# Performance work log

Hardware: AMD Instinct MI355X
Metric: run time of the kernel (lower is better)

Reference implementation:

```python
import jax, jax.numpy as jnp
import numpy as np

WS = 8          # window size
DIM = 512       # channels
NH = 16         # heads
HD = DIM // NH  # head dim = 32
N = WS * WS     # tokens per window = 64
NW = 64         # windows per image
B = 16          # images
BW = B * NW     # total windows = 1024
SCALE = HD ** -0.5


def _relative_position_index():
    # Swin relative position index, shape (N, N), values in [0, (2*WS-1)^2)
    coords = np.stack(np.meshgrid(np.arange(WS), np.arange(WS), indexing='ij'))  # (2, WS, WS)
    coords_flat = coords.reshape(2, -1)                                           # (2, N)
    rel = coords_flat[:, :, None] - coords_flat[:, None, :]                       # (2, N, N)
    rel = rel.transpose(1, 2, 0).astype(np.int32)                                 # (N, N, 2)
    rel[:, :, 0] += WS - 1
    rel[:, :, 1] += WS - 1
    rel[:, :, 0] *= 2 * WS - 1
    return jnp.asarray(rel.sum(-1))                                               # (N, N)


def setup_inputs() -> dict:
    key = jax.random.key(0)
    ks = jax.random.split(key, 7)
    x = jax.random.normal(ks[0], (BW, N, DIM), dtype=jnp.float32)
    mask = jax.random.normal(ks[1], (NW, N, N), dtype=jnp.float32)  # shift mask (additive)
    qkv_w = jax.random.normal(ks[2], (3 * DIM, DIM), dtype=jnp.float32) * 0.02
    qkv_b = jax.random.normal(ks[3], (3 * DIM,), dtype=jnp.float32) * 0.02
    rel_bias_table = jax.random.normal(ks[4], ((2 * WS - 1) ** 2, NH), dtype=jnp.float32) * 0.02
    proj_w = jax.random.normal(ks[5], (DIM, DIM), dtype=jnp.float32) * 0.02
    proj_b = jax.random.normal(ks[6], (DIM,), dtype=jnp.float32) * 0.02
    rel_index = _relative_position_index()
    return {"x": x, "mask": mask, "qkv_w": qkv_w, "qkv_b": qkv_b,
            "rel_bias_table": rel_bias_table, "proj_w": proj_w, "proj_b": proj_b,
            "rel_index": rel_index}


def reference(x, mask, qkv_w, qkv_b, rel_bias_table, proj_w, proj_b, rel_index):
    # qkv projection: (BW, N, 3*DIM) -> (3, BW, NH, N, HD)
    qkv = (x @ qkv_w.T + qkv_b).reshape(BW, N, 3, NH, HD).transpose(2, 0, 3, 1, 4)
    q, k, v = qkv[0], qkv[1], qkv[2]
    # scaled dot-product scores: (BW, NH, N, N)
    attn = jnp.einsum('bhnd,bhmd->bhnm', q * SCALE, k)
    # relative position bias: gather (N*N,) -> (N, N, NH) -> (NH, N, N)
    bias = rel_bias_table[rel_index.reshape(-1)].reshape(N, N, NH).transpose(2, 0, 1)
    attn = attn + bias[None]
    # shift mask: broadcast over images and heads
    attn = attn.reshape(B, NW, NH, N, N) + mask[None, :, None]
    attn = jax.nn.softmax(attn.reshape(BW, NH, N, N), axis=-1)
    # weighted values: (BW, NH, N, HD) -> (BW, N, DIM)
    out = jnp.einsum('bhnm,bhmd->bhnd', attn, v).transpose(0, 2, 1, 3).reshape(BW, N, DIM)
    return out @ proj_w.T + proj_b
```

## Files before the change

kernel.cpp:

```cpp
#include <hip/hip_runtime.h>
#include <hip/hip_bf16.h>

typedef __bf16 bf16;
typedef __bf16 bf16x4 __attribute__((ext_vector_type(4)));
typedef __bf16 bf16x8 __attribute__((ext_vector_type(8)));
typedef float  f32x4  __attribute__((ext_vector_type(4)));

#define AS1 __attribute__((address_space(1)))
#define AS3 __attribute__((address_space(3)))

__device__ __forceinline__ void gld_lds16(const void* g, void* l) {
    __builtin_amdgcn_global_load_lds((AS1 void*)g, (AS3 void*)l, 16, 0, 0);
}

__global__ void cvt_kernel(const float* __restrict__ in, bf16* __restrict__ out,
                           int n4) {
    for (long i = (long)blockIdx.x * blockDim.x + threadIdx.x; i < n4;
         i += (long)gridDim.x * blockDim.x) {
        f32x4 v = ((const f32x4*)in)[i];
        bf16x4 h;
#pragma unroll
        for (int e = 0; e < 4; ++e) h[e] = (bf16)v[e];
        ((bf16x4*)out)[i] = h;
    }
}

__global__ void bias_kernel(const int* __restrict__ rel_index,
                            const float* __restrict__ table,
                            float* __restrict__ bias) {
    int idx = blockIdx.x * 256 + threadIdx.x;
    int rc = idx & 4095;
    int h  = idx >> 12;
    bias[idx] = table[rel_index[rc] * 16 + h];
}

#define STAGE(GBASE, LBASE, SK0)                                          \
    { _Pragma("unroll")                                                   \
      for (int c_ = 0; c_ < 2; ++c_)                                      \
          gld_lds16((GBASE) + c_ * 16 * 512 + (SK0),                      \
                    (LBASE) + (w * 2 + c_) * 512); }

#define PHASE(S, KK, IH, LOADB, GB, LB, SK0, VM)                            \
  {                                                                         \
    const bf16* ap_ = sA + ((S)*2+(KK))*8192 + (wm128+(IH)*64+r16)*32 + cq8;\
    _Pragma("unroll")                                                       \
    for (int ii = 0; ii < 4; ++ii) av[ii] = *(const bf16x8*)(ap_ + ii*512); \
    if (LOADB) {                                                            \
      const bf16* bp_ = sB + ((S)*2+(KK))*8192 + (wn64+r16)*32 + cq8;       \
      _Pragma("unroll")                                                     \
      for (int jj = 0; jj < 4; ++jj) bv[jj] = *(const bf16x8*)(bp_+jj*512); \
    }                                                                       \
    STAGE(GB, LB, SK0);                                                     \
    __builtin_amdgcn_sched_barrier(0);                                      \
    __builtin_amdgcn_s_barrier();                                           \
    asm volatile("s_waitcnt lgkmcnt(0)");                                   \
    __builtin_amdgcn_sched_barrier(0);                                      \
    __builtin_amdgcn_s_setprio(1);                                          \
    _Pragma("unroll")                                                       \
    for (int ii = 0; ii < 4; ++ii)                                          \
      _Pragma("unroll")                                                     \
      for (int jj = 0; jj < 4; ++jj)                                        \
        acc[(IH)*4+ii][jj] = __builtin_amdgcn_mfma_f32_16x16x32_bf16(       \
            av[ii], bv[jj], acc[(IH)*4+ii][jj], 0, 0, 0);                   \
    __builtin_amdgcn_s_setprio(0);                                          \
    if (VM) asm volatile("s_waitcnt vmcnt(4)");                             \
    __builtin_amdgcn_sched_barrier(0);                                      \
    __builtin_amdgcn_s_barrier();                                           \
  }

#define GEMM_PREAMBLE                                                       \
    __shared__ __attribute__((aligned(16))) char smemraw[131072];           \
    bf16* sA = (bf16*)smemraw;                                              \
    bf16* sB = sA + 32768;                                                  \
    const int t     = threadIdx.x;                                          \
    const int w     = t >> 6;                                               \
    const int lane  = t & 63;                                               \
    const int q     = lane >> 4;                                            \
    const int r16   = lane & 15;                                            \
    const int wm128 = (w >> 2) * 128;                                       \
    const int wn64  = (w & 3) * 64;                                         \
    const int sc8   = (((lane & 3) ^ ((lane >> 2) & 3)) << 3);              \
    const int cq8   = ((q ^ (r16 & 3)) << 3);

#define GEMM_MAIN(ABASE, BBASE)                                             \
    const bf16* Ast = (ABASE) + (bM + w * 32 + (lane >> 2)) * 512 + sc8;    \
    const bf16* Bst = (BBASE) + (bN + w * 32 + (lane >> 2)) * 512 + sc8;    \
    f32x4 acc[8][4];                                                        \
    _Pragma("unroll")                                                       \
    for (int i = 0; i < 8; ++i)                                             \
        _Pragma("unroll")                                                   \
        for (int j = 0; j < 4; ++j) acc[i][j] = f32x4{0.f, 0.f, 0.f, 0.f};  \
    bf16x8 av[4], bv[4];                                                    \
    STAGE(Ast, sA + 0,     0);                                              \
    STAGE(Bst, sB + 0,     0);                                              \
    STAGE(Ast, sA + 8192,  32);                                             \
    STAGE(Bst, sB + 8192,  32);                                             \
    STAGE(Ast, sA + 16384, 64);                                             \
    STAGE(Bst, sB + 16384, 64);                                             \
    asm volatile("s_waitcnt vmcnt(4)");                                     \
    __builtin_amdgcn_sched_barrier(0);                                      \
    __builtin_amdgcn_s_barrier();                                           \
    for (int i = 0; i < 4; ++i) {                                           \
        const int t1 = 2 * i + 1;                                           \
        const int t2 = (2 * i + 2 < 8) ? 2 * i + 2 : 7;                     \
        const int t3 = (2 * i + 3 < 8) ? 2 * i + 3 : 7;                     \
        PHASE(0, 0, 0, 1, Ast, sA + 24576, t1 * 64 + 32, 0)                 \
        PHASE(0, 0, 1, 0, Bst, sB + 24576, t1 * 64 + 32, 0)                 \
        PHASE(0, 1, 1, 1, Ast, sA + 0,     t2 * 64,      0)                 \
        PHASE(0, 1, 0, 0, Bst, sB + 0,     t2 * 64,      1)                 \
        PHASE(1, 0, 0, 1, Ast, sA + 8192,  t2 * 64 + 32, 0)                 \
        PHASE(1, 0, 1, 0, Bst, sB + 8192,  t2 * 64 + 32, 0)                 \
        PHASE(1, 1, 1, 1, Ast, sA + 16384, t3 * 64,      0)                 \
        PHASE(1, 1, 0, 0, Bst, sB + 16384, t3 * 64,      1)                 \
    }                                                                       \
    asm volatile("s_waitcnt vmcnt(0)");                                     \
    __builtin_amdgcn_sched_barrier(0);                                      \
    __builtin_amdgcn_s_barrier();

__global__ __launch_bounds__(512, 2) void gemm1_qkv8(
    const bf16* __restrict__ A, const bf16* __restrict__ B,
    const float* __restrict__ bias, bf16* __restrict__ Cq,
    bf16* __restrict__ Ckv)
{
    GEMM_PREAMBLE
    const int bid = blockIdx.x;
    const int wg  = (bid & 7) * 192 + (bid >> 3);
    const long bM = (long)(wg / 6) * 256;
    const long bN = (long)(wg % 6) * 256;

    GEMM_MAIN(A, B)

    const bool isQ = (bN < 512);
    const float sc = isQ ? 0.17677669529663687f : 1.0f;
    bf16* ct = (bf16*)smemraw;
#pragma unroll
    for (int j = 0; j < 4; ++j) {
        const int col  = wn64 + j * 16 + r16;
        const float bvv = bias[bN + col];
        const int chunk = col >> 3, cl = col & 7;
#pragma unroll
        for (int i = 0; i < 8; ++i)
#pragma unroll
            for (int r = 0; r < 4; ++r) {
                const int row = wm128 + i * 16 + q * 4 + r;
                ct[row * 256 + ((chunk ^ ((row >> 2) & 7)) << 3) + cl] =
                    (bf16)((acc[i][j][r] + bvv) * sc);
            }
    }
    __syncthreads();

    bf16* __restrict__ outp = isQ ? (Cq + bM * 512 + bN)
                                  : (Ckv + bM * 1024 + (bN - 512));
    const int ostr = isQ ? 512 : 1024;
#pragma unroll
    for (int it = 0; it < 16; ++it) {
        const int row = w * 32 + it * 2 + (lane >> 5);
        const int c   = lane & 31;
        uint4 v = *(const uint4*)(ct + row * 256 +
                                  ((c ^ ((row >> 2) & 7)) << 3));
        *(uint4*)(outp + (long)row * ostr + c * 8) = v;
    }
}

__global__ __launch_bounds__(512, 2) void gemm2_proj8(
    const bf16* __restrict__ A, const bf16* __restrict__ B,
    const float* __restrict__ bias, float* __restrict__ C)
{
    GEMM_PREAMBLE
    const int bid = blockIdx.x;
    const int wg  = (bid & 7) * 64 + (bid >> 3);
    const long bM = (long)(wg >> 1) * 256;
    const long bN = (long)(wg & 1) * 256;

    GEMM_MAIN(A, B)

#pragma unroll
    for (int j = 0; j < 4; ++j) {
        const long col = bN + wn64 + j * 16 + r16;
        const float bvv = bias[col];
#pragma unroll
        for (int i = 0; i < 8; ++i) {
            const long row = bM + wm128 + i * 16 + q * 4;
#pragma unroll
            for (int r = 0; r < 4; ++r)
                C[(row + r) * 512L + col] = acc[i][j][r] + bvv;
        }
    }
}

__global__ __launch_bounds__(256) void attn_kernel4(
    bf16* __restrict__ qbuf, const bf16* __restrict__ kv,
    const float* __restrict__ mask, const float* __restrict__ bias)
{
    __shared__ __attribute__((aligned(16))) bf16 smem[24576];
    const int t    = threadIdx.x;
    const int wv   = t >> 6;
    const int lane = t & 63;
    const int q    = lane >> 4;
    const int r16  = lane & 15;
    const int bw   = blockIdx.x >> 2;
    const int hg   = blockIdx.x & 3;
    const int h    = hg * 4 + wv;
    const int nw   = bw & 63;
    const long rowbase = (long)bw * 64;

    bf16* Qs = smem + wv * 6144;
    bf16* Ks = Qs + 2048;
    bf16* Vt = Qs + 4096;
    bf16* Ps = Qs;

    const int sc8 = (((lane & 3) ^ ((lane >> 2) & 3)) << 3);
#pragma unroll
    for (int it = 0; it < 4; ++it) {
        const int tok = it * 16 + (lane >> 2);
        gld_lds16(qbuf + (rowbase + tok) * 512  + h * 32 + sc8, Qs + it * 512);
        gld_lds16(kv   + (rowbase + tok) * 1024 + h * 32 + sc8, Ks + it * 512);
    }
    {
        const bf16* gv = kv + (rowbase + lane) * 1024 + 512 + h * 32;
        uint4 vtmp[4];
#pragma unroll
        for (int jj = 0; jj < 4; ++jj) vtmp[jj] = ((const uint4*)gv)[jj];
        const bf16* vrow = (const bf16*)vtmp;
        const int tchunk = lane >> 3, tin = lane & 7;
#pragma unroll
        for (int hd = 0; hd < 32; ++hd)
            Vt[hd * 64 + ((tchunk ^ (hd & 7)) << 3) + tin] = vrow[hd];
    }
    asm volatile("s_waitcnt vmcnt(0)" ::: "memory");

    const int cq8 = ((q ^ (r16 & 3)) << 3);
    f32x4 acc[4][4];
    {
        bf16x8 av[4], bv[4];
#pragma unroll
        for (int ti = 0; ti < 4; ++ti)
            av[ti] = *(const bf16x8*)&Qs[(ti * 16 + r16) * 32 + cq8];
#pragma unroll
        for (int tj = 0; tj < 4; ++tj)
            bv[tj] = *(const bf16x8*)&Ks[(tj * 16 + r16) * 32 + cq8];
        const f32x4 z = f32x4{0.f, 0.f, 0.f, 0.f};
#pragma unroll
        for (int ti = 0; ti < 4; ++ti)
#pragma unroll
            for (int tj = 0; tj < 4; ++tj)
                acc[ti][tj] = __builtin_amdgcn_mfma_f32_16x16x32_bf16(
                    av[ti], bv[tj], z, 0, 0, 0);
    }

    const float LOG2E  = 1.4426950408889634f;
    const float* biasH = bias + h * 4096;
    const float* maskW = mask + nw * 4096;

#pragma unroll
    for (int ti = 0; ti < 4; ++ti) {
#pragma unroll
        for (int r = 0; r < 4; ++r) {
            const int row = ti * 16 + q * 4 + r;
            float mx = -1e30f;
#pragma unroll
            for (int tj = 0; tj < 4; ++tj) {
                const int col = tj * 16 + r16;
                float s = acc[ti][tj][r]
                        + biasH[row * 64 + col] + maskW[row * 64 + col];
                acc[ti][tj][r] = s;
                mx = fmaxf(mx, s);
            }
#pragma unroll
            for (int d = 1; d < 16; d <<= 1)
                mx = fmaxf(mx, __shfl_xor(mx, d, 16));
            float sum = 0.f;
#pragma unroll
            for (int tj = 0; tj < 4; ++tj) {
                float e = exp2f((acc[ti][tj][r] - mx) * LOG2E);
                acc[ti][tj][r] = e;
                sum += e;
            }
#pragma unroll
            for (int d = 1; d < 16; d <<= 1)
                sum += __shfl_xor(sum, d, 16);
            const float inv = 1.0f / sum;
#pragma unroll
            for (int tj = 0; tj < 4; ++tj) {
                const int c = tj * 16 + r16;
                Ps[row * 64 + ((((c >> 3) ^ (row & 7)) << 3) + (c & 7))] =
                    (bf16)(acc[ti][tj][r] * inv);
            }
        }
    }

    f32x4 o[4][2];
#pragma unroll
    for (int ti = 0; ti < 4; ++ti)
#pragma unroll
        for (int tn = 0; tn < 2; ++tn)
            o[ti][tn] = f32x4{0.f, 0.f, 0.f, 0.f};

#pragma unroll
    for (int ks = 0; ks < 2; ++ks) {
        bf16x8 av[4], bv[2];
        const int ch = (((ks * 4 + q) ^ (r16 & 7)) << 3);
#pragma unroll
        for (int ti = 0; ti < 4; ++ti)
            av[ti] = *(const bf16x8*)&Ps[(ti * 16 + r16) * 64 + ch];
#pragma unroll
        for (int tn = 0; tn < 2; ++tn)
            bv[tn] = *(const bf16x8*)&Vt[(tn * 16 + r16) * 64 + ch];
#pragma unroll
        for (int ti = 0; ti < 4; ++ti)
#pragma unroll
            for (int tn = 0; tn < 2; ++tn)
                o[ti][tn] = __builtin_amdgcn_mfma_f32_16x16x32_bf16(
                    av[ti], bv[tn], o[ti][tn], 0, 0, 0);
    }

#pragma unroll
    for (int ti = 0; ti < 4; ++ti)
#pragma unroll
        for (int tn = 0; tn < 2; ++tn)
#pragma unroll
            for (int r = 0; r < 4; ++r)
                Qs[(ti * 16 + q * 4 + r) * 32 + tn * 16 + r16] =
                    (bf16)(o[ti][tn][r]);
    __syncthreads();

    bf16* op = qbuf + rowbase * 512 + hg * 128;
#pragma unroll
    for (int it = 0; it < 4; ++it) {
        const int idx = it * 256 + t;
        const int row = idx >> 4;
        const int c   = idx & 15;
        const int hl  = c >> 2;
        uint4 v = *(const uint4*)(smem + hl * 6144 + row * 32 + (c & 3) * 8);
        *(uint4*)(op + (long)row * 512 + hl * 32 + (c & 3) * 8) = v;
    }
}

extern "C" void kernel_launch(void* const* d_in, const int* in_sizes, int n_in,
                              void* d_out, int out_size, void* d_ws, size_t ws_size,
                              hipStream_t stream) {
    const float* x      = (const float*)d_in[0];
    const float* mask   = (const float*)d_in[1];
    const float* qkv_w  = (const float*)d_in[2];
    const float* qkv_b  = (const float*)d_in[3];
    const float* table  = (const float*)d_in[4];
    const float* proj_w = (const float*)d_in[5];
    const float* proj_b = (const float*)d_in[6];
    const int*   relidx = (const int*)d_in[7];
    float* out = (float*)d_out;

    char*  ws   = (char*)d_ws;
    float* bias = (float*)ws;
    bf16*  qbuf = (bf16*)(ws + 262144);
    bf16*  xbf  = (bf16*)(ws + 67371008);
    bf16*  wq   = (bf16*)(ws + 134479872);
    bf16*  wp   = (bf16*)(ws + 136052736);
    const size_t need_full = 136577024ull + 134217728ull;
    bf16* kvbuf = (ws_size >= need_full) ? (bf16*)(ws + 136577024)
                                         : (bf16*)d_out;

    bias_kernel<<<256, 256, 0, stream>>>(relidx, table, bias);
    cvt_kernel<<<2048, 256, 0, stream>>>(x,      xbf, 8388608);
    cvt_kernel<<<768,  256, 0, stream>>>(qkv_w,  wq,  196608);
    cvt_kernel<<<256,  256, 0, stream>>>(proj_w, wp,  65536);

    gemm1_qkv8<<<1536, 512, 0, stream>>>(xbf, wq, qkv_b, qbuf, kvbuf);
    attn_kernel4<<<4096, 256, 0, stream>>>(qbuf, kvbuf, mask, bias);
    gemm2_proj8<<<512, 512, 0, stream>>>(qbuf, wp, proj_b, out);
}
```

Measured before the change: 534.7 us.

## Double-buffer LDS fragment registers and change LDS swizzle pattern in GEMMs

Restructures the GEMM main loop so each phase prefetches the next A/B fragments from LDS into alternate register buffers while MFMAs consume the previous ones. Partial lgkmcnt and adjusted vmcnt waits let LDS reads and global-to-LDS loads overlap with compute. It also changes the XOR swizzle for the staged tiles in both the GEMM and the attention kernel, aiming to reduce LDS bank conflicts. The cost is more VGPRs for the duplicated fragments and more delicate wait-count correctness.

After: 538.2 us. Within noise of the previous version (+0.7%).

```diff
diff --git a/kernel.cpp b/kernel.cpp
--- a/kernel.cpp
+++ b/kernel.cpp
@@ -40,33 +40,38 @@
           gld_lds16((GBASE) + c_ * 16 * 512 + (SK0),                      \
                     (LBASE) + (w * 2 + c_) * 512); }
 
-#define PHASE(S, KK, IH, LOADB, GB, LB, SK0, VM)                            \
-  {                                                                         \
-    const bf16* ap_ = sA + ((S)*2+(KK))*8192 + (wm128+(IH)*64+r16)*32 + cq8;\
+#define FRAG_A(DST, S, KK, IH)                                              \
+  { const bf16* ap_ = sA + ((S)*2+(KK))*8192 + (wm128+(IH)*64+r16)*32 + cq8;\
     _Pragma("unroll")                                                       \
-    for (int ii = 0; ii < 4; ++ii) av[ii] = *(const bf16x8*)(ap_ + ii*512); \
-    if (LOADB) {                                                            \
-      const bf16* bp_ = sB + ((S)*2+(KK))*8192 + (wn64+r16)*32 + cq8;       \
-      _Pragma("unroll")                                                     \
-      for (int jj = 0; jj < 4; ++jj) bv[jj] = *(const bf16x8*)(bp_+jj*512); \
-    }                                                                       \
+    for (int ii_ = 0; ii_ < 4; ++ii_)                                       \
+        DST[ii_] = *(const bf16x8*)(ap_ + ii_*512); }
+
+#define FRAG_B(DST, S, KK)                                                  \
+  { const bf16* bp_ = sB + ((S)*2+(KK))*8192 + (wn64+r16)*32 + cq8;         \
+    _Pragma("unroll")                                                       \
+    for (int jj_ = 0; jj_ < 4; ++jj_)                                       \
+        DST[jj_] = *(const bf16x8*)(bp_ + jj_*512); }
+
+#define PH(PFAD, PFS, PFKK, PFIH, PFB, PFBD, GB, LB, SK0, LGK, UAV, UBV,    \
+           UIH, VMA)                                                        \
+  { FRAG_A(PFAD, PFS, PFKK, PFIH);                                          \
+    if (PFB) FRAG_B(PFBD, PFS, PFKK);                                       \
     STAGE(GB, LB, SK0);                                                     \
     __builtin_amdgcn_sched_barrier(0);                                      \
     __builtin_amdgcn_s_barrier();                                           \
-    asm volatile("s_waitcnt lgkmcnt(0)");                                   \
+    asm volatile("s_waitcnt lgkmcnt(" #LGK ")");                            \
     __builtin_amdgcn_sched_barrier(0);                                      \
     __builtin_amdgcn_s_setprio(1);                                          \
     _Pragma("unroll")                                                       \
-    for (int ii = 0; ii < 4; ++ii)                                          \
+    for (int ii_ = 0; ii_ < 4; ++ii_)                                       \
       _Pragma("unroll")                                                     \
-      for (int jj = 0; jj < 4; ++jj)                                        \
-        acc[(IH)*4+ii][jj] = __builtin_amdgcn_mfma_f32_16x16x32_bf16(       \
-            av[ii], bv[jj], acc[(IH)*4+ii][jj], 0, 0, 0);                   \
+      for (int jj_ = 0; jj_ < 4; ++jj_)                                     \
+        acc[(UIH)*4+ii_][jj_] = __builtin_amdgcn_mfma_f32_16x16x32_bf16(    \
+            UAV[ii_], UBV[jj_], acc[(UIH)*4+ii_][jj_], 0, 0, 0);            \
     __builtin_amdgcn_s_setprio(0);                                          \
-    if (VM) asm volatile("s_waitcnt vmcnt(4)");                             \
-    __builtin_amdgcn_sched_barrier(0);                                      \
-    __builtin_amdgcn_s_barrier();                                           \
-  }
+    asm volatile(VMA);                                                      \
+    __builtin_amdgcn_sched_barrier(0);                                      \
+    __builtin_amdgcn_s_barrier(); }
 
 #define GEMM_PREAMBLE                                                       \
     __shared__ __attribute__((aligned(16))) char smemraw[131072];           \
@@ -79,8 +84,8 @@
     const int r16   = lane & 15;                                            \
     const int wm128 = (w >> 2) * 128;                                       \
     const int wn64  = (w & 3) * 64;                                         \
-    const int sc8   = (((lane & 3) ^ ((lane >> 2) & 3)) << 3);              \
-    const int cq8   = ((q ^ (r16 & 3)) << 3);
+    const int sc8   = (((lane & 3) ^ ((lane >> 4) & 3)) << 3);              \
+    const int cq8   = ((q ^ ((r16 >> 2) & 3)) << 3);
 
 #define GEMM_MAIN(ABASE, BBASE)                                             \
     const bf16* Ast = (ABASE) + (bM + w * 32 + (lane >> 2)) * 512 + sc8;    \
@@ -90,7 +95,7 @@
     for (int i = 0; i < 8; ++i)                                             \
         _Pragma("unroll")                                                   \
         for (int j = 0; j < 4; ++j) acc[i][j] = f32x4{0.f, 0.f, 0.f, 0.f};  \
-    bf16x8 av[4], bv[4];                                                    \
+    bf16x8 avA[4], avB[4], bvA[4], bvB[4];                                  \
     STAGE(Ast, sA + 0,     0);                                              \
     STAGE(Bst, sB + 0,     0);                                              \
     STAGE(Ast, sA + 8192,  32);                                             \
@@ -100,20 +105,26 @@
     asm volatile("s_waitcnt vmcnt(4)");                                     \
     __builtin_amdgcn_sched_barrier(0);                                      \
     __builtin_amdgcn_s_barrier();                                           \
+    FRAG_A(avA, 0, 0, 0);                                                   \
+    FRAG_B(bvA, 0, 0);                                                      \
     for (int i = 0; i < 4; ++i) {                                           \
         const int t1 = 2 * i + 1;                                           \
         const int t2 = (2 * i + 2 < 8) ? 2 * i + 2 : 7;                     \
         const int t3 = (2 * i + 3 < 8) ? 2 * i + 3 : 7;                     \
-        PHASE(0, 0, 0, 1, Ast, sA + 24576, t1 * 64 + 32, 0)                 \
-        PHASE(0, 0, 1, 0, Bst, sB + 24576, t1 * 64 + 32, 0)                 \
-        PHASE(0, 1, 1, 1, Ast, sA + 0,     t2 * 64,      0)                 \
-        PHASE(0, 1, 0, 0, Bst, sB + 0,     t2 * 64,      1)                 \
-        PHASE(1, 0, 0, 1, Ast, sA + 8192,  t2 * 64 + 32, 0)                 \
-        PHASE(1, 0, 1, 0, Bst, sB + 8192,  t2 * 64 + 32, 0)                 \
-        PHASE(1, 1, 1, 1, Ast, sA + 16384, t3 * 64,      0)                 \
-        PHASE(1, 1, 0, 0, Bst, sB + 16384, t3 * 64,      1)                 \
+        PH(avB,0,0,1, 0,bvB, Ast, sA+24576, t1*64+32, 4, avA,bvA,0, "")     \
+        PH(avA,0,1,1, 1,bvB, Bst, sB+24576, t1*64+32, 8, avB,bvA,1, "")     \
+        PH(avB,0,1,0, 0,bvA, Ast, sA+0,     t2*64,    4, avA,bvB,1,         \
+           "s_waitcnt vmcnt(6)")                                            \
+        PH(avA,1,0,0, 1,bvA, Bst, sB+0,     t2*64,    8, avB,bvB,0, "")     \
+        PH(avB,1,0,1, 0,bvB, Ast, sA+8192,  t2*64+32, 4, avA,bvA,0,         \
+           "s_waitcnt vmcnt(6)")                                            \
+        PH(avA,1,1,1, 1,bvB, Bst, sB+8192,  t2*64+32, 8, avB,bvA,1, "")     \
+        PH(avB,1,1,0, 0,bvA, Ast, sA+16384, t3*64,    4, avA,bvB,1,         \
+           "s_waitcnt vmcnt(6)")                                            \
+        PH(avA,0,0,0, 1,bvA, Bst, sB+16384, t3*64,    8, avB,bvB,0,         \
+           "s_waitcnt vmcnt(4)")                                            \
     }                                                                       \
-    asm volatile("s_waitcnt vmcnt(0)");                                     \
+    asm volatile("s_waitcnt vmcnt(0) lgkmcnt(0)");                          \
     __builtin_amdgcn_sched_barrier(0);                                      \
     __builtin_amdgcn_s_barrier();
 
@@ -209,7 +220,7 @@
     bf16* Vt = Qs + 4096;
     bf16* Ps = Qs;
 
-    const int sc8 = (((lane & 3) ^ ((lane >> 2) & 3)) << 3);
+    const int sc8 = (((lane & 3) ^ ((lane >> 4) & 3)) << 3);
 #pragma unroll
     for (int it = 0; it < 4; ++it) {
         const int tok = it * 16 + (lane >> 2);
@@ -229,7 +240,7 @@
     }
     asm volatile("s_waitcnt vmcnt(0)" ::: "memory");
 
-    const int cq8 = ((q ^ (r16 & 3)) << 3);
+    const int cq8 = ((q ^ ((r16 >> 2) & 3)) << 3);
     f32x4 acc[4][4];
     {
         bf16x8 av[4], bv[4];
```
